# Kernel optimization log

Measured on AMD Instinct MI355X. Metric: run time of the kernel, lower is better.

The kernel has to match this reference:

```python
import jax, jax.numpy as jnp
import numpy as np
from jax import lax

STRIDES = (4, 8, 16, 32, 64)
SIZES = (32, 64, 128, 256, 512)
RATIOS = (0.5, 1.0, 2.0)
IMG_H, IMG_W = 1024, 1024
PRE_NMS = 1000
POST_NMS = 1000
NMS_THRESH = 0.7
BBOX_CLIP = float(np.log(1000.0 / 16.0))
NEG_INF = -1e9


def _cell_anchors(size):
    a = []
    for r in RATIOS:
        w = size * np.sqrt(1.0 / r)
        h = size * np.sqrt(r)
        a.append([-w / 2.0, -h / 2.0, w / 2.0, h / 2.0])
    return np.array(a, np.float32)  # [A,4]


def _level_anchors(H, W, stride, size):
    cell = _cell_anchors(size)  # [A,4]
    ys = np.arange(H, dtype=np.float32) * stride
    xs = np.arange(W, dtype=np.float32) * stride
    yy, xx = np.meshgrid(ys, xs, indexing='ij')  # row-major (H,W)
    shifts = np.stack([xx, yy, xx, yy], axis=-1).reshape(-1, 1, 4)
    return jnp.asarray((shifts + cell[None]).reshape(-1, 4))  # [(H*W*A),4] in (H,W,A) order


def conv2d(x, w, b, pad):
    y = lax.conv_general_dilated(x, w, (1, 1), pad,
                                 dimension_numbers=('NCHW', 'OIHW', 'NCHW'))
    return y + b[None, :, None, None]


def decode(deltas, anchors):
    widths = anchors[:, 2] - anchors[:, 0] + 1.0
    heights = anchors[:, 3] - anchors[:, 1] + 1.0
    ctr_x = anchors[:, 0] + 0.5 * widths
    ctr_y = anchors[:, 1] + 0.5 * heights
    dx, dy = deltas[..., 0], deltas[..., 1]
    dw = jnp.minimum(deltas[..., 2], BBOX_CLIP)
    dh = jnp.minimum(deltas[..., 3], BBOX_CLIP)
    pcx = dx * widths + ctr_x
    pcy = dy * heights + ctr_y
    pw = jnp.exp(dw) * widths
    ph = jnp.exp(dh) * heights
    return jnp.stack([pcx - 0.5 * pw, pcy - 0.5 * ph,
                      pcx + 0.5 * pw - 1.0, pcy + 0.5 * ph - 1.0], axis=-1)


def iou_matrix(boxes):
    area = (boxes[:, 2] - boxes[:, 0]) * (boxes[:, 3] - boxes[:, 1])
    lt = jnp.maximum(boxes[:, None, :2], boxes[None, :, :2])
    rb = jnp.minimum(boxes[:, None, 2:], boxes[None, :, 2:])
    wh = jnp.maximum(rb - lt, 0.0)
    inter = wh[..., 0] * wh[..., 1]
    return inter / (area[:, None] + area[None, :] - inter + 1e-9)


def nms_keep(boxes):
    # boxes [N,4] already sorted by score desc; greedy NMS -> bool keep mask
    N = boxes.shape[0]
    iou = iou_matrix(boxes)

    def body(keep, i):
        row = jnp.take(iou, i, axis=0) > NMS_THRESH
        row = row.at[i].set(False)
        keep = jnp.where(keep[i], keep & ~row, keep)
        return keep, None

    keep, _ = lax.scan(body, jnp.ones((N,), bool), jnp.arange(N))
    return keep


def _forward(feats, conv_w, conv_b, cls_w, cls_b, bbox_w, bbox_b):
    level_boxes, level_scores = [], []
    for lvl, feat in enumerate(feats):
        B, _, H, W = feat.shape
        t = jax.nn.relu(conv2d(feat, conv_w, conv_b, 'SAME'))
        logits = conv2d(t, cls_w, cls_b, 'VALID')    # [B,A,H,W]
        breg = conv2d(t, bbox_w, bbox_b, 'VALID')    # [B,4A,H,W]
        A = logits.shape[1]
        scores = jnp.transpose(logits, (0, 2, 3, 1)).reshape(B, -1)            # (H,W,A)
        deltas = breg.reshape(B, A, 4, H, W).transpose(0, 3, 4, 1, 2).reshape(B, -1, 4)
        anchors = _level_anchors(H, W, STRIDES[lvl], SIZES[lvl])
        boxes = decode(deltas, anchors)  # [B,N,4]
        boxes = jnp.stack([jnp.clip(boxes[..., 0], 0.0, IMG_W - 1.0),
                           jnp.clip(boxes[..., 1], 0.0, IMG_H - 1.0),
                           jnp.clip(boxes[..., 2], 0.0, IMG_W - 1.0),
                           jnp.clip(boxes[..., 3], 0.0, IMG_H - 1.0)], axis=-1)
        k = min(PRE_NMS, scores.shape[1])
        top_s, idx = lax.top_k(scores, k)                                   # [B,k]
        top_b = jnp.take_along_axis(boxes, idx[..., None], axis=1)          # [B,k,4]
        keep = jax.vmap(nms_keep)(top_b)                                    # [B,k] bool
        level_scores.append(jnp.where(keep, top_s, NEG_INF))
        level_boxes.append(top_b)
    all_s = jnp.concatenate(level_scores, axis=1)
    all_b = jnp.concatenate(level_boxes, axis=1)
    fs, fi = lax.top_k(all_s, POST_NMS)                                     # [B,POST]
    fb = jnp.take_along_axis(all_b, fi[..., None], axis=1)                  # [B,POST,4]
    return jnp.concatenate([fb, fs[..., None]], axis=-1)                    # [B,POST,5]


def setup_inputs() -> dict:
    key = jax.random.key(0)
    ks = jax.random.split(key, 8)
    C = 256
    feats = {
        'feat0': jax.random.normal(ks[0], (2, C, 256, 256), jnp.float32),
        'feat1': jax.random.normal(ks[1], (2, C, 128, 128), jnp.float32),
        'feat2': jax.random.normal(ks[2], (2, C, 64, 64), jnp.float32),
        'feat3': jax.random.normal(ks[3], (2, C, 32, 32), jnp.float32),
        'feat4': jax.random.normal(ks[4], (2, C, 16, 16), jnp.float32),
    }
    params = {
        'conv_w': jax.random.normal(ks[5], (C, C, 3, 3), jnp.float32) * 0.01,
        'conv_b': jnp.zeros((C,), jnp.float32),
        'cls_w': jax.random.normal(ks[6], (3, C, 1, 1), jnp.float32) * 0.01,
        'cls_b': jnp.zeros((3,), jnp.float32),
        'bbox_w': jax.random.normal(ks[7], (12, C, 1, 1), jnp.float32) * 0.01,
        'bbox_b': jnp.zeros((12,), jnp.float32),
    }
    return {**feats, **params}


def reference(feat0, feat1, feat2, feat3, feat4, conv_w, conv_b, cls_w, cls_b, bbox_w, bbox_b):
    return _forward([feat0, feat1, feat2, feat3, feat4],
                    conv_w, conv_b, cls_w, cls_b, bbox_w, bbox_b)
```

## Files before the change

kernel.cpp:

```cpp
#include <hip/hip_runtime.h>
#include <cmath>


#define NTOT_PER_IMG 261888
#define ATOT_PER_IMG 4768

__constant__ int c_NLVL[5] = {196608, 49152, 12288, 3072, 768};
__constant__ int c_KLVL[5] = {1000, 1000, 1000, 1000, 768};
__constant__ int c_LOFF[5] = {0, 196608, 245760, 258048, 261120};
__constant__ int c_AOFF[5] = {0, 1000, 2000, 3000, 4000};

struct Anch { float cx1[3]; float cy1[3]; };
struct ConvCfg { Anch an[5]; };

__device__ __forceinline__ void gl16(const float* g, float* l) {
  __builtin_amdgcn_global_load_lds(
      (const __attribute__((address_space(1))) void*)g,
      (__attribute__((address_space(3))) void*)l, 16, 0, 0);
}

__global__ __launch_bounds__(256) void wtrans(const float* __restrict__ Wsrc,
                                              float* __restrict__ Wt) {
  __shared__ float T[16][17];
  int k0 = blockIdx.x * 16;
  int o0 = blockIdx.y * 16;
  int i = threadIdx.x >> 4, j = threadIdx.x & 15;
  T[i][j] = Wsrc[(size_t)(o0 + i) * 2304 + (k0 + j)];
  __syncthreads();
  Wt[(size_t)(k0 + i) * 256 + (o0 + j)] = T[j][i];
}

__global__ __launch_bounds__(256, 2) void conv_gemm(
    const float* __restrict__ f0, const float* __restrict__ f1,
    const float* __restrict__ f2, const float* __restrict__ f3,
    const float* __restrict__ f4, const float* __restrict__ Wt,
    const float* __restrict__ convb, const float* __restrict__ clsw,
    const float* __restrict__ clsb, const float* __restrict__ bboxw,
    const float* __restrict__ bboxb, float* __restrict__ scoresOut,
    float4* __restrict__ boxesOut, ConvCfg cfg) {
  __shared__ __align__(16) float s_mem[5424];
  __shared__ float s_Red2[272];
  float* const s_w = s_mem;
  float* const s_x = s_mem + 4608;
  float* const s_tl = s_mem;

  int b = blockIdx.x;
  const float* feat;
  int lvl, img, tile, H, logW, stride, lvlOff;
  if (b < 2048) {
    lvl = 0; feat = f0; H = 256; logW = 8; stride = 4; lvlOff = 0;
    img = b >> 10; tile = b & 1023;
  } else if (b < 2560) {
    lvl = 1; feat = f1; H = 128; logW = 7; stride = 8; lvlOff = 196608;
    int r = b - 2048; img = r >> 8; tile = r & 255;
  } else if (b < 2688) {
    lvl = 2; feat = f2; H = 64; logW = 6; stride = 16; lvlOff = 245760;
    int r = b - 2560; img = r >> 6; tile = r & 63;
  } else if (b < 2720) {
    lvl = 3; feat = f3; H = 32; logW = 5; stride = 32; lvlOff = 258048;
    int r = b - 2688; img = r >> 4; tile = r & 15;
  } else {
    lvl = 4; feat = f4; H = 16; logW = 4; stride = 64; lvlOff = 261120;
    int r = b - 2720; img = r >> 2; tile = r & 3;
  }
  const int W = H, HW = H * W;
  const int p0 = tile * 64;
  const float* fimg = feat + (size_t)img * 256 * HW;

  const int log2nc = (logW < 6) ? logW : 6;
  const int ncols = 1 << log2nc;
  const int R = 64 >> log2nc;
  const int py0 = p0 >> logW;
  const int c_start = p0 & (W - 1);
  const int WIN = ncols + 2;
  const int NX = (R + 2) * WIN;

  const int tid = threadIdx.x;
  const int oc0 = (tid >> 3) * 8;
  const int pxg = tid & 7;
  const int px0 = pxg * 8;
  const int trow = px0 >> log2nc;
  const int tcol0 = px0 & (ncols - 1);

  int goffX = -1, loffX = -1;
  if (tid < NX) {
    int lr = tid / WIN;
    int lc = tid - lr * WIN;
    int sy = py0 - 1 + lr;
    int sx = c_start - 1 + lc;
    loffX = lr * 68 + lc;
    if (sy >= 0 && sy < H && sx >= 0 && sx < W) goffX = sy * W + sx;
  }

  float acc[8][8];
#pragma unroll
  for (int i = 0; i < 8; i++)
#pragma unroll
    for (int p = 0; p < 8; p++) acc[i][p] = 0.f;

  const int t4 = tid << 2;

  {
    gl16(Wt + t4, s_w + t4);
    gl16(Wt + 1024 + t4, s_w + 1024 + t4);
    if (tid < 64) gl16(Wt + 2048 + t4, s_w + 2048 + t4);
    if (loffX >= 0) s_x[loffX] = (goffX >= 0) ? fimg[goffX] : 0.f;
  }
  __syncthreads();

#pragma unroll 1
  for (int ic = 0; ic < 256; ic++) {
    const float* wb = s_w + (ic & 1) * 2304;
    const float* xb = s_x + (ic & 1) * 408;

    float pxv;
    if (ic < 255) {
      const float* wg = Wt + (size_t)(ic + 1) * 2304;
      float* wn = s_w + ((ic + 1) & 1) * 2304;
      gl16(wg + t4, wn + t4);
      gl16(wg + 1024 + t4, wn + 1024 + t4);
      if (tid < 64) gl16(wg + 2048 + t4, wn + 2048 + t4);
      const float* fnext = fimg + (size_t)(ic + 1) * HW;
      pxv = (goffX >= 0) ? fnext[goffX] : 0.f;
    }

#pragma unroll 1
    for (int ky = 0; ky < 3; ky++) {
      const float* xr = xb + (trow + ky) * 68 + tcol0;
      float4 xA = *(const float4*)(xr);
      float4 xB = *(const float4*)(xr + 4);
      float2 xC = *(const float2*)(xr + 8);
      float xw[10] = {xA.x, xA.y, xA.z, xA.w,
                      xB.x, xB.y, xB.z, xB.w, xC.x, xC.y};
      const float* wky = wb + ky * 768 + oc0;
#pragma unroll
      for (int kx = 0; kx < 3; kx++) {
        float4 wa = *(const float4*)(wky + kx * 256);
        float4 wc = *(const float4*)(wky + kx * 256 + 4);
        float wv[8] = {wa.x, wa.y, wa.z, wa.w, wc.x, wc.y, wc.z, wc.w};
#pragma unroll
        for (int i = 0; i < 8; i++)
#pragma unroll
          for (int p = 0; p < 8; p++)
            acc[i][p] = __builtin_fmaf(wv[i], xw[p + kx], acc[i][p]);
      }
    }

    if (ic < 255) {
      float* xn = s_x + ((ic + 1) & 1) * 408;
      if (loffX >= 0) xn[loffX] = pxv;
    }
    __syncthreads();
  }

  float cb[8];
#pragma unroll
  for (int i = 0; i < 8; i++) cb[i] = convb[oc0 + i];

  const Anch an = cfg.an[lvl];
  const float BCLIP = (float)4.135166556742356;
  const size_t obase = (size_t)img * NTOT_PER_IMG + lvlOff;

#pragma unroll 1
  for (int r = 0; r < 4; r++) {
    if ((pxg >> 1) == r) {
      int pl = px0 - 16 * r;
#pragma unroll
      for (int p = 0; p < 8; p++) {
        float4 v0 = make_float4(fmaxf(acc[0][p] + cb[0], 0.f),
                                fmaxf(acc[1][p] + cb[1], 0.f),
                                fmaxf(acc[2][p] + cb[2], 0.f),
                                fmaxf(acc[3][p] + cb[3], 0.f));
        float4 v1 = make_float4(fmaxf(acc[4][p] + cb[4], 0.f),
                                fmaxf(acc[5][p] + cb[5], 0.f),
                                fmaxf(acc[6][p] + cb[6], 0.f),
                                fmaxf(acc[7][p] + cb[7], 0.f));
        *(float4*)(s_tl + (pl + p) * 260 + oc0) = v0;
        *(float4*)(s_tl + (pl + p) * 260 + oc0 + 4) = v1;
      }
    }
    __syncthreads();

    if (tid < 240) {
      int px = tid / 15, c = tid - px * 15;
      const float* wr0 = (c < 3) ? (clsw + c * 256) : (bboxw + (c - 3) * 256);
      float bb = (c < 3) ? clsb[c] : bboxb[c - 3];
      const float* trow2 = &s_tl[px * 260];
      float tot = 0.f;
#pragma unroll
      for (int g = 0; g < 16; g++) {
        const float* wr = wr0 + g * 16;
        const float* tr = trow2 + g * 16;
        float s = 0.f;
#pragma unroll
        for (int i = 0; i < 16; i++) s += wr[i] * tr[i];
        tot += s;
      }
      s_Red2[px * 17 + c] = tot + bb;
    }
    __syncthreads();

    if (tid < 48) {
      int px = tid / 3, a = tid - px * 3;
      int pxl = p0 + r * 16 + px;
      int gy = pxl >> logW, gx = pxl & (W - 1);
      float sc = s_Red2[px * 17 + a];
      float dxv = s_Red2[px * 17 + 3 + a * 4 + 0];
      float dyv = s_Red2[px * 17 + 3 + a * 4 + 1];
      float dwv = s_Red2[px * 17 + 3 + a * 4 + 2];
      float dhv = s_Red2[px * 17 + 3 + a * 4 + 3];
      float sx = (float)(gx * stride), sy = (float)(gy * stride);
      float x1 = __fadd_rn(sx, an.cx1[a]);
      float x2 = __fsub_rn(sx, an.cx1[a]);
      float y1 = __fadd_rn(sy, an.cy1[a]);
      float y2 = __fsub_rn(sy, an.cy1[a]);
      float wdt = __fadd_rn(__fsub_rn(x2, x1), 1.0f);
      float hgt = __fadd_rn(__fsub_rn(y2, y1), 1.0f);
      float ctx = __fadd_rn(x1, __fmul_rn(0.5f, wdt));
      float cty = __fadd_rn(y1, __fmul_rn(0.5f, hgt));
      float dw = fminf(dwv, BCLIP), dh = fminf(dhv, BCLIP);
      float pcx = __fadd_rn(__fmul_rn(dxv, wdt), ctx);
      float pcy = __fadd_rn(__fmul_rn(dyv, hgt), cty);
      float pw = __fmul_rn(expf(dw), wdt);
      float ph = __fmul_rn(expf(dh), hgt);
      float hw = __fmul_rn(0.5f, pw), hh = __fmul_rn(0.5f, ph);
      float bx1 = __fsub_rn(pcx, hw);
      float by1 = __fsub_rn(pcy, hh);
      float bx2 = __fsub_rn(__fadd_rn(pcx, hw), 1.0f);
      float by2 = __fsub_rn(__fadd_rn(pcy, hh), 1.0f);
      bx1 = fminf(fmaxf(bx1, 0.f), 1023.f);
      by1 = fminf(fmaxf(by1, 0.f), 1023.f);
      bx2 = fminf(fmaxf(bx2, 0.f), 1023.f);
      by2 = fminf(fmaxf(by2, 0.f), 1023.f);
      size_t o = obase + (size_t)pxl * 3 + a;
      scoresOut[o] = sc;
      boxesOut[o] = make_float4(bx1, by1, bx2, by2);
    }
    __syncthreads();
  }
}

__device__ __forceinline__ unsigned fkeyu(unsigned b) {
  return (b & 0x80000000u) ? ~b : (b | 0x80000000u);
}
__device__ __forceinline__ unsigned fkey(float f) {
  return fkeyu(__float_as_uint(f));
}
__device__ __forceinline__ float funkey(unsigned u) {
  unsigned b = (u & 0x80000000u) ? (u & 0x7fffffffu) : ~u;
  return __uint_as_float(b);
}

template <bool FINAL>
__global__ __launch_bounds__(1024) void topk_kernel(
    const float* __restrict__ scoresIn, const float4* __restrict__ boxesIn,
    float* __restrict__ scoresOut, float4* __restrict__ boxesOut,
    float* __restrict__ finalOut) {
  __shared__ unsigned long long keys[1024];
  __shared__ unsigned hist[256 * 16];
  __shared__ unsigned s_hsum[256];
  __shared__ unsigned s_comm[4];
  int lvl = 0, img, N, k;
  const float* src;
  const float4* bsrc;
  if (FINAL) {
    img = blockIdx.x; N = ATOT_PER_IMG; k = 1000;
    src = scoresIn + (size_t)img * ATOT_PER_IMG;
    bsrc = boxesIn + (size_t)img * ATOT_PER_IMG;
  } else {
    lvl = blockIdx.x; img = blockIdx.y;
    N = c_NLVL[lvl]; k = c_KLVL[lvl];
    src = scoresIn + (size_t)img * NTOT_PER_IMG + c_LOFF[lvl];
    bsrc = boxesIn + (size_t)img * NTOT_PER_IMG + c_LOFF[lvl];
  }
  const int tid = threadIdx.x;
  const int rep = tid & 15;
  const uint4* src4 = (const uint4*)src;
  const int N4 = N >> 2;

  unsigned pref = 0, pmask = 0, krem = (unsigned)k, cntT = 0;
  for (int pass = 3; pass >= 0; pass--) {
    int shift = pass * 8;
    for (int z = tid; z < 4096; z += 1024) hist[z] = 0;
    __syncthreads();
    for (int i = tid; i < N4; i += 1024) {
      uint4 v = src4[i];
      unsigned u0 = fkeyu(v.x), u1 = fkeyu(v.y);
      unsigned u2 = fkeyu(v.z), u3 = fkeyu(v.w);
      if ((u0 & pmask) == pref)
        atomicAdd(&hist[((u0 >> shift) & 255) * 16 + rep], 1u);
      if ((u1 & pmask) == pref)
        atomicAdd(&hist[((u1 >> shift) & 255) * 16 + rep], 1u);
      if ((u2 & pmask) == pref)
        atomicAdd(&hist[((u2 >> shift) & 255) * 16 + rep], 1u);
      if ((u3 & pmask) == pref)
        atomicAdd(&hist[((u3 >> shift) & 255) * 16 + rep], 1u);
    }
    __syncthreads();
    if (tid < 256) {
      unsigned s = 0;
#pragma unroll
      for (int r2 = 0; r2 < 16; r2++) s += hist[tid * 16 + r2];
      s_hsum[tid] = s;
    }
    __syncthreads();
    if (tid == 0) {
      unsigned cum = 0;
      for (int d = 255; d >= 0; d--) {
        unsigned c = s_hsum[d];
        if (cum + c >= krem) {
          s_comm[0] = krem - cum; s_comm[1] = c; s_comm[2] = (unsigned)d;
          break;
        }
        cum += c;
      }
    }
    __syncthreads();
    krem = s_comm[0]; cntT = s_comm[1];
    pref |= s_comm[2] << shift;
    pmask |= 0xFFu << shift;
    __syncthreads();
  }
  const unsigned T = pref, r = krem;
  unsigned m = (unsigned)N;
  if (r < cntT) {
    unsigned lo = 0, hi = (unsigned)N;
    while (lo < hi) {
      unsigned mid = (lo + hi) >> 1;
      if (tid == 0) s_comm[3] = 0;
      __syncthreads();
      for (unsigned i = tid; i < mid; i += 1024)
        if (fkey(src[i]) == T) atomicAdd(&s_comm[3], 1u);
      __syncthreads();
      unsigned c = s_comm[3];
      __syncthreads();
      if (c >= r) hi = mid; else lo = mid + 1;
    }
    m = lo;
  }
  if (tid == 0) s_comm[3] = 0;
  __syncthreads();
  for (int i = tid; i < N4; i += 1024) {
    uint4 v = src4[i];
#pragma unroll
    for (int j = 0; j < 4; j++) {
      unsigned bu = (j == 0) ? v.x : (j == 1) ? v.y : (j == 2) ? v.z : v.w;
      unsigned u = fkeyu(bu);
      unsigned idx = (unsigned)(i * 4 + j);
      if (u > T || (u == T && idx < m)) {
        unsigned p = atomicAdd(&s_comm[3], 1u);
        if (p < 1024)
          keys[p] = ((unsigned long long)u << 32) | (unsigned)(~idx);
      }
    }
  }
  __syncthreads();
  if (tid >= k) keys[tid] = 0ull;
  __syncthreads();
  for (unsigned k2 = 2; k2 <= 1024; k2 <<= 1) {
    for (unsigned j = k2 >> 1; j > 0; j >>= 1) {
      unsigned i = tid, ixj = i ^ j;
      if (ixj > i) {
        unsigned long long a = keys[i], b = keys[ixj];
        bool sw = ((i & k2) == 0) ? (a < b) : (a > b);
        if (sw) { keys[i] = b; keys[ixj] = a; }
      }
      __syncthreads();
    }
  }
  if (tid < k) {
    unsigned long long key = keys[tid];
    unsigned u = (unsigned)(key >> 32);
    unsigned idx = ~((unsigned)key);
    float sc = funkey(u);
    float4 b = bsrc[idx];
    if (FINAL) {
      float* o = finalOut + ((size_t)img * 1000 + tid) * 5;
      o[0] = b.x; o[1] = b.y; o[2] = b.z; o[3] = b.w; o[4] = sc;
    } else {
      scoresOut[(size_t)img * ATOT_PER_IMG + c_AOFF[lvl] + tid] = sc;
      boxesOut[(size_t)img * ATOT_PER_IMG + c_AOFF[lvl] + tid] = b;
    }
  }
}

__global__ __launch_bounds__(256) void nms_matrix(
    const float4* __restrict__ allb, unsigned long long* __restrict__ supp) {
  int lvl = blockIdx.x, img = blockIdx.y, rb = blockIdx.z;
  int k = c_KLVL[lvl];
  int task = img * 5 + lvl;
  const float4* src = allb + (size_t)img * ATOT_PER_IMG + c_AOFF[lvl];
  __shared__ float4 bb[1000];
  __shared__ float ar[1000];
  for (int j = threadIdx.x; j < k; j += 256) {
    float4 b = src[j];
    bb[j] = b;
    ar[j] = __fmul_rn(__fsub_rn(b.z, b.x), __fsub_rn(b.w, b.y));
  }
  __syncthreads();
  int i = rb * 256 + threadIdx.x;
  if (i < k) {
    float4 bi = bb[i];
    float ai = ar[i];
    unsigned long long* row = supp + ((size_t)task * 1024 + i) * 16;
    int jw0 = i >> 6;
    for (int jw = 0; jw < jw0; jw++) row[jw] = 0ull;
    for (int jw = jw0; jw < 16; jw++) {
      unsigned long long bits = 0;
      int jbase = jw * 64;
      for (int jj = 0; jj < 64; jj++) {
        int j = jbase + jj;
        if (j > i && j < k) {
          float4 bj = bb[j];
          float ltx = fmaxf(bi.x, bj.x), lty = fmaxf(bi.y, bj.y);
          float rbx = fminf(bi.z, bj.z), rby = fminf(bi.w, bj.w);
          float wx = fmaxf(__fsub_rn(rbx, ltx), 0.f);
          float wy = fmaxf(__fsub_rn(rby, lty), 0.f);
          float inter = __fmul_rn(wx, wy);
          float den = __fadd_rn(__fsub_rn(__fadd_rn(ai, ar[j]), inter), 1e-9f);
          if (__fdiv_rn(inter, den) > 0.7f) bits |= 1ull << jj;
        }
      }
      row[jw] = bits;
    }
  }
}

__global__ __launch_bounds__(64) void nms_scan(
    const float* __restrict__ topS, const unsigned long long* __restrict__ supp,
    float* __restrict__ fscore) {
  int lvl = blockIdx.x, img = blockIdx.y;
  int k = c_KLVL[lvl];
  int task = img * 5 + lvl;
  int lane = threadIdx.x;
  const unsigned long long* base = supp + (size_t)task * 1024 * 16;
  unsigned long long rem = 0, keep = 0;
  for (int b0 = 0; b0 < k; b0 += 16) {
    unsigned long long buf[16];
#pragma unroll
    for (int t = 0; t < 16; t++) {
      int i = b0 + t;
      buf[t] = (lane < 16 && i < k) ? base[(size_t)i * 16 + lane] : 0ull;
    }
#pragma unroll
    for (int t = 0; t < 16; t++) {
      int i = b0 + t;
      if (i >= k) break;
      int wi = i >> 6, bi = i & 63;
      unsigned long long rw = __shfl(rem, wi);
      if (!((rw >> bi) & 1ull)) {
        rem |= buf[t];
        if (lane == wi) keep |= (1ull << bi);
      }
    }
  }
  const float* ts = topS + (size_t)img * ATOT_PER_IMG + c_AOFF[lvl];
  float* fs = fscore + (size_t)img * ATOT_PER_IMG + c_AOFF[lvl];
  for (int i = lane; i < k; i += 64) {
    int wi = i >> 6;
    unsigned long long kw = __shfl(keep, wi);
    fs[i] = ((kw >> (i & 63)) & 1ull) ? ts[i] : -1e9f;
  }
}

static Anch mkAnch(double size) {
  Anch a;
  const double R[3] = {0.5, 1.0, 2.0};
  for (int i = 0; i < 3; i++) {
    double w = size * sqrt(1.0 / R[i]);
    double h = size * sqrt(R[i]);
    a.cx1[i] = (float)(-w / 2.0);
    a.cy1[i] = (float)(-h / 2.0);
  }
  return a;
}

extern "C" void kernel_launch(void* const* d_in, const int* in_sizes, int n_in,
                              void* d_out, int out_size, void* d_ws,
                              size_t ws_size, hipStream_t stream) {
  (void)in_sizes; (void)n_in; (void)out_size; (void)ws_size;
  const float* f0 = (const float*)d_in[0];
  const float* f1 = (const float*)d_in[1];
  const float* f2 = (const float*)d_in[2];
  const float* f3 = (const float*)d_in[3];
  const float* f4 = (const float*)d_in[4];
  const float* conv_w = (const float*)d_in[5];
  const float* conv_b = (const float*)d_in[6];
  const float* cls_w  = (const float*)d_in[7];
  const float* cls_b  = (const float*)d_in[8];
  const float* bbox_w = (const float*)d_in[9];
  const float* bbox_b = (const float*)d_in[10];
  float* out = (float*)d_out;

  float* wsf = (float*)d_ws;
  float* Wt     = wsf;
  float* scores = Wt + 589824;
  float* boxes  = scores + 2 * NTOT_PER_IMG;
  float* topS   = boxes + (size_t)2 * NTOT_PER_IMG * 4;
  float* allb   = topS + 2 * ATOT_PER_IMG;
  float* fscore = allb + (size_t)2 * ATOT_PER_IMG * 4;
  unsigned long long* supp =
      (unsigned long long*)(fscore + 2 * ATOT_PER_IMG);

  wtrans<<<dim3(144, 16), 256, 0, stream>>>(conv_w, Wt);

  ConvCfg cfg;
  const double SZ[5] = {32, 64, 128, 256, 512};
  for (int l = 0; l < 5; l++) cfg.an[l] = mkAnch(SZ[l]);

  conv_gemm<<<2728, 256, 0, stream>>>(f0, f1, f2, f3, f4, Wt, conv_b, cls_w,
                                      cls_b, bbox_w, bbox_b, scores,
                                      (float4*)boxes, cfg);

  topk_kernel<false><<<dim3(5, 2), 1024, 0, stream>>>(
      scores, (const float4*)boxes, topS, (float4*)allb, nullptr);
  nms_matrix<<<dim3(5, 2, 4), 256, 0, stream>>>((const float4*)allb, supp);
  nms_scan<<<dim3(5, 2), 64, 0, stream>>>(topS, supp, fscore);
  topk_kernel<true><<<2, 1024, 0, stream>>>(
      fscore, (const float4*)allb, nullptr, nullptr, out);
}
```

Measured before the change: 3.203 ms.

## Split per-level top-k into chunked local selection plus merge pass

The per-level radix top-k, previously one 1024-thread block per level and image (10 blocks), becomes a two-stage selection. Level 0 is split into 8 chunks and level 1 into 2, giving 26 blocks that each select a local top-1000 into a candidate buffer. A merge kernel then runs radix select on those candidates per level. The aim is to spread the large level-0 scan over more CUs, at the cost of an extra launch and a candidate buffer round trip through global memory.

After: 3.232 ms. About the same (+0.9%).

```diff
diff --git a/kernel.cpp b/kernel.cpp
--- a/kernel.cpp
+++ b/kernel.cpp
@@ -4,11 +4,24 @@
 
 #define NTOT_PER_IMG 261888
 #define ATOT_PER_IMG 4768
+#define CAND_PER_IMG 12768
 
 __constant__ int c_NLVL[5] = {196608, 49152, 12288, 3072, 768};
 __constant__ int c_KLVL[5] = {1000, 1000, 1000, 1000, 768};
 __constant__ int c_LOFF[5] = {0, 196608, 245760, 258048, 261120};
 __constant__ int c_AOFF[5] = {0, 1000, 2000, 3000, 4000};
+
+__constant__ int cA_lvl[13]   = {0,0,0,0,0,0,0,0,1,1,2,3,4};
+__constant__ int cA_start[13] = {0,24576,49152,73728,98304,122880,147456,
+                                 172032,0,24576,0,0,0};
+__constant__ int cA_N[13]     = {24576,24576,24576,24576,24576,24576,24576,
+                                 24576,24576,24576,12288,3072,768};
+__constant__ int cA_k[13]     = {1000,1000,1000,1000,1000,1000,1000,1000,
+                                 1000,1000,1000,1000,768};
+__constant__ int cA_out[13]   = {0,1000,2000,3000,4000,5000,6000,7000,
+                                 8000,9000,10000,11000,12000};
+__constant__ int cB_N[5]    = {8000,2000,1000,1000,768};
+__constant__ int cB_base[5] = {0,8000,10000,11000,12000};
 
 struct Anch { float cx1[3]; float cy1[3]; };
 struct ConvCfg { Anch an[5]; };
@@ -251,28 +264,17 @@
   return __uint_as_float(b);
 }
 
-template <bool FINAL>
-__global__ __launch_bounds__(1024) void topk_kernel(
-    const float* __restrict__ scoresIn, const float4* __restrict__ boxesIn,
-    float* __restrict__ scoresOut, float4* __restrict__ boxesOut,
-    float* __restrict__ finalOut) {
-  __shared__ unsigned long long keys[1024];
+__global__ __launch_bounds__(1024) void topk_local(
+    const float* __restrict__ scoresIn, unsigned long long* __restrict__ cand) {
   __shared__ unsigned hist[256 * 16];
   __shared__ unsigned s_hsum[256];
   __shared__ unsigned s_comm[4];
-  int lvl = 0, img, N, k;
-  const float* src;
-  const float4* bsrc;
-  if (FINAL) {
-    img = blockIdx.x; N = ATOT_PER_IMG; k = 1000;
-    src = scoresIn + (size_t)img * ATOT_PER_IMG;
-    bsrc = boxesIn + (size_t)img * ATOT_PER_IMG;
-  } else {
-    lvl = blockIdx.x; img = blockIdx.y;
-    N = c_NLVL[lvl]; k = c_KLVL[lvl];
-    src = scoresIn + (size_t)img * NTOT_PER_IMG + c_LOFF[lvl];
-    bsrc = boxesIn + (size_t)img * NTOT_PER_IMG + c_LOFF[lvl];
-  }
+  const int cid = blockIdx.x, img = blockIdx.y;
+  const int lvl = cA_lvl[cid];
+  const int N = cA_N[cid], k = cA_k[cid], start = cA_start[cid];
+  const float* src =
+      scoresIn + (size_t)img * NTOT_PER_IMG + c_LOFF[lvl] + start;
+  unsigned long long* outp = cand + (size_t)img * CAND_PER_IMG + cA_out[cid];
   const int tid = threadIdx.x;
   const int rep = tid & 15;
   const uint4* src4 = (const uint4*)src;
@@ -346,12 +348,97 @@
     for (int j = 0; j < 4; j++) {
       unsigned bu = (j == 0) ? v.x : (j == 1) ? v.y : (j == 2) ? v.z : v.w;
       unsigned u = fkeyu(bu);
-      unsigned idx = (unsigned)(i * 4 + j);
-      if (u > T || (u == T && idx < m)) {
+      unsigned lidx = (unsigned)(i * 4 + j);
+      if (u > T || (u == T && lidx < m)) {
         unsigned p = atomicAdd(&s_comm[3], 1u);
-        if (p < 1024)
-          keys[p] = ((unsigned long long)u << 32) | (unsigned)(~idx);
-      }
+        outp[p] = ((unsigned long long)u << 32) |
+                  (unsigned)(~(unsigned)(start + lidx));
+      }
+    }
+  }
+}
+
+__global__ __launch_bounds__(1024) void topk_merge(
+    const unsigned long long* __restrict__ cand,
+    const float4* __restrict__ boxesIn, float* __restrict__ scoresOut,
+    float4* __restrict__ boxesOut) {
+  __shared__ unsigned long long keys[1024];
+  __shared__ unsigned hist[256 * 16];
+  __shared__ unsigned s_hsum[256];
+  __shared__ unsigned s_comm[4];
+  const int lvl = blockIdx.x, img = blockIdx.y;
+  const int N = cB_N[lvl], k = c_KLVL[lvl];
+  const unsigned levelN = (unsigned)c_NLVL[lvl];
+  const unsigned long long* src = cand + (size_t)img * CAND_PER_IMG +
+                                  cB_base[lvl];
+  const float4* bsrc = boxesIn + (size_t)img * NTOT_PER_IMG + c_LOFF[lvl];
+  const int tid = threadIdx.x;
+  const int rep = tid & 15;
+
+  unsigned pref = 0, pmask = 0, krem = (unsigned)k, cntT = 0;
+  for (int pass = 3; pass >= 0; pass--) {
+    int shift = pass * 8;
+    for (int z = tid; z < 4096; z += 1024) hist[z] = 0;
+    __syncthreads();
+    for (int i = tid; i < N; i += 1024) {
+      unsigned u = (unsigned)(src[i] >> 32);
+      if ((u & pmask) == pref)
+        atomicAdd(&hist[((u >> shift) & 255) * 16 + rep], 1u);
+    }
+    __syncthreads();
+    if (tid < 256) {
+      unsigned s = 0;
+#pragma unroll
+      for (int r2 = 0; r2 < 16; r2++) s += hist[tid * 16 + r2];
+      s_hsum[tid] = s;
+    }
+    __syncthreads();
+    if (tid == 0) {
+      unsigned cum = 0;
+      for (int d = 255; d >= 0; d--) {
+        unsigned c = s_hsum[d];
+        if (cum + c >= krem) {
+          s_comm[0] = krem - cum; s_comm[1] = c; s_comm[2] = (unsigned)d;
+          break;
+        }
+        cum += c;
+      }
+    }
+    __syncthreads();
+    krem = s_comm[0]; cntT = s_comm[1];
+    pref |= s_comm[2] << shift;
+    pmask |= 0xFFu << shift;
+    __syncthreads();
+  }
+  const unsigned T = pref, r = krem;
+  unsigned m = levelN;
+  if (r < cntT) {
+    unsigned lo = 0, hi = levelN;
+    while (lo < hi) {
+      unsigned mid = (lo + hi) >> 1;
+      if (tid == 0) s_comm[3] = 0;
+      __syncthreads();
+      for (int i = tid; i < N; i += 1024) {
+        unsigned long long kv = src[i];
+        if ((unsigned)(kv >> 32) == T && (~(unsigned)kv) < mid)
+          atomicAdd(&s_comm[3], 1u);
+      }
+      __syncthreads();
+      unsigned c = s_comm[3];
+      __syncthreads();
+      if (c >= r) hi = mid; else lo = mid + 1;
+    }
+    m = lo;
+  }
+  if (tid == 0) s_comm[3] = 0;
+  __syncthreads();
+  for (int i = tid; i < N; i += 1024) {
+    unsigned long long kv = src[i];
+    unsigned u = (unsigned)(kv >> 32);
+    unsigned idx = ~(unsigned)kv;
+    if (u > T || (u == T && idx < m)) {
+      unsigned p = atomicAdd(&s_comm[3], 1u);
+      if (p < 1024) keys[p] = kv;
     }
   }
   __syncthreads();
@@ -374,13 +461,125 @@
     unsigned idx = ~((unsigned)key);
     float sc = funkey(u);
     float4 b = bsrc[idx];
-    if (FINAL) {
-      float* o = finalOut + ((size_t)img * 1000 + tid) * 5;
-      o[0] = b.x; o[1] = b.y; o[2] = b.z; o[3] = b.w; o[4] = sc;
-    } else {
-      scoresOut[(size_t)img * ATOT_PER_IMG + c_AOFF[lvl] + tid] = sc;
-      boxesOut[(size_t)img * ATOT_PER_IMG + c_AOFF[lvl] + tid] = b;
-    }
+    scoresOut[(size_t)img * ATOT_PER_IMG + c_AOFF[lvl] + tid] = sc;
+    boxesOut[(size_t)img * ATOT_PER_IMG + c_AOFF[lvl] + tid] = b;
+  }
+}
+
+__global__ __launch_bounds__(1024) void topk_final(
+    const float* __restrict__ scoresIn, const float4* __restrict__ boxesIn,
+    float* __restrict__ finalOut) {
+  __shared__ unsigned long long keys[1024];
+  __shared__ unsigned hist[256 * 16];
+  __shared__ unsigned s_hsum[256];
+  __shared__ unsigned s_comm[4];
+  const int img = blockIdx.x;
+  const int N = ATOT_PER_IMG, k = 1000;
+  const float* src = scoresIn + (size_t)img * ATOT_PER_IMG;
+  const float4* bsrc = boxesIn + (size_t)img * ATOT_PER_IMG;
+  const int tid = threadIdx.x;
+  const int rep = tid & 15;
+  const uint4* src4 = (const uint4*)src;
+  const int N4 = N >> 2;
+
+  unsigned pref = 0, pmask = 0, krem = (unsigned)k, cntT = 0;
+  for (int pass = 3; pass >= 0; pass--) {
+    int shift = pass * 8;
+    for (int z = tid; z < 4096; z += 1024) hist[z] = 0;
+    __syncthreads();
+    for (int i = tid; i < N4; i += 1024) {
+      uint4 v = src4[i];
+      unsigned u0 = fkeyu(v.x), u1 = fkeyu(v.y);
+      unsigned u2 = fkeyu(v.z), u3 = fkeyu(v.w);
+      if ((u0 & pmask) == pref)
+        atomicAdd(&hist[((u0 >> shift) & 255) * 16 + rep], 1u);
+      if ((u1 & pmask) == pref)
+        atomicAdd(&hist[((u1 >> shift) & 255) * 16 + rep], 1u);
+      if ((u2 & pmask) == pref)
+        atomicAdd(&hist[((u2 >> shift) & 255) * 16 + rep], 1u);
+      if ((u3 & pmask) == pref)
+        atomicAdd(&hist[((u3 >> shift) & 255) * 16 + rep], 1u);
+    }
+    __syncthreads();
+    if (tid < 256) {
+      unsigned s = 0;
+#pragma unroll
+      for (int r2 = 0; r2 < 16; r2++) s += hist[tid * 16 + r2];
+      s_hsum[tid] = s;
+    }
+    __syncthreads();
+    if (tid == 0) {
+      unsigned cum = 0;
+      for (int d = 255; d >= 0; d--) {
+        unsigned c = s_hsum[d];
+        if (cum + c >= krem) {
+          s_comm[0] = krem - cum; s_comm[1] = c; s_comm[2] = (unsigned)d;
+          break;
+        }
+        cum += c;
+      }
+    }
+    __syncthreads();
+    krem = s_comm[0]; cntT = s_comm[1];
+    pref |= s_comm[2] << shift;
+    pmask |= 0xFFu << shift;
+    __syncthreads();
+  }
+  const unsigned T = pref, r = krem;
+  unsigned m = (unsigned)N;
+  if (r < cntT) {
+    unsigned lo = 0, hi = (unsigned)N;
+    while (lo < hi) {
+      unsigned mid = (lo + hi) >> 1;
+      if (tid == 0) s_comm[3] = 0;
+      __syncthreads();
+      for (unsigned i = tid; i < mid; i += 1024)
+        if (fkey(src[i]) == T) atomicAdd(&s_comm[3], 1u);
+      __syncthreads();
+      unsigned c = s_comm[3];
+      __syncthreads();
+      if (c >= r) hi = mid; else lo = mid + 1;
+    }
+    m = lo;
+  }
+  if (tid == 0) s_comm[3] = 0;
+  __syncthreads();
+  for (int i = tid; i < N4; i += 1024) {
+    uint4 v = src4[i];
+#pragma unroll
+    for (int j = 0; j < 4; j++) {
+      unsigned bu = (j == 0) ? v.x : (j == 1) ? v.y : (j == 2) ? v.z : v.w;
+      unsigned u = fkeyu(bu);
+      unsigned idx = (unsigned)(i * 4 + j);
+      if (u > T || (u == T && idx < m)) {
+        unsigned p = atomicAdd(&s_comm[3], 1u);
+        if (p < 1024)
+          keys[p] = ((unsigned long long)u << 32) | (unsigned)(~idx);
+      }
+    }
+  }
+  __syncthreads();
+  if (tid >= k) keys[tid] = 0ull;
+  __syncthreads();
+  for (unsigned k2 = 2; k2 <= 1024; k2 <<= 1) {
+    for (unsigned j = k2 >> 1; j > 0; j >>= 1) {
+      unsigned i = tid, ixj = i ^ j;
+      if (ixj > i) {
+        unsigned long long a = keys[i], b = keys[ixj];
+        bool sw = ((i & k2) == 0) ? (a < b) : (a > b);
+        if (sw) { keys[i] = b; keys[ixj] = a; }
+      }
+      __syncthreads();
+    }
+  }
+  if (tid < k) {
+    unsigned long long key = keys[tid];
+    unsigned u = (unsigned)(key >> 32);
+    unsigned idx = ~((unsigned)key);
+    float sc = funkey(u);
+    float4 b = bsrc[idx];
+    float* o = finalOut + ((size_t)img * 1000 + tid) * 5;
+    o[0] = b.x; o[1] = b.y; o[2] = b.z; o[3] = b.w; o[4] = sc;
   }
 }
 
@@ -501,6 +700,7 @@
   float* fscore = allb + (size_t)2 * ATOT_PER_IMG * 4;
   unsigned long long* supp =
       (unsigned long long*)(fscore + 2 * ATOT_PER_IMG);
+  unsigned long long* cand = supp + (size_t)10 * 1024 * 16;
 
   wtrans<<<dim3(144, 16), 256, 0, stream>>>(conv_w, Wt);
 
@@ -512,10 +712,10 @@
                                       cls_b, bbox_w, bbox_b, scores,
                                       (float4*)boxes, cfg);
 
-  topk_kernel<false><<<dim3(5, 2), 1024, 0, stream>>>(
-      scores, (const float4*)boxes, topS, (float4*)allb, nullptr);
+  topk_local<<<dim3(13, 2), 1024, 0, stream>>>(scores, cand);
+  topk_merge<<<dim3(5, 2), 1024, 0, stream>>>(cand, (const float4*)boxes,
+                                              topS, (float4*)allb);
   nms_matrix<<<dim3(5, 2, 4), 256, 0, stream>>>((const float4*)allb, supp);
   nms_scan<<<dim3(5, 2), 64, 0, stream>>>(topS, supp, fscore);
-  topk_kernel<true><<<2, 1024, 0, stream>>>(
-      fscore, (const float4*)allb, nullptr, nullptr, out);
-}
+  topk_final<<<2, 1024, 0, stream>>>(fscore, (const float4*)allb, out);
+}
```
